# Optimization experiments

Hardware: AMD Instinct MI355X
Metric: run time of the kernel (lower is better)

The kernel has to match this reference:

```python
import jax, jax.numpy as jnp
import numpy as np

HIDDEN = 2048
N_HEADS = 16
N_KV_HEADS = 4
HEAD_DIM = HIDDEN // N_HEADS  # 128
WINDOW = 2048
ROPE_THETA = 10000.0


def setup_inputs() -> dict:
    key = jax.random.key(0)
    ks = jax.random.split(key, 5)
    B, S = 1, 4096
    scale = 0.02
    return {
        "hidden_states": jax.random.normal(ks[0], (B, S, HIDDEN), dtype=jnp.float32),
        # nn.Linear weights are [out_features, in_features]
        "q_w": jax.random.normal(ks[1], (N_HEADS * HEAD_DIM, HIDDEN), dtype=jnp.float32) * scale,
        "k_w": jax.random.normal(ks[2], (N_KV_HEADS * HEAD_DIM, HIDDEN), dtype=jnp.float32) * scale,
        "v_w": jax.random.normal(ks[3], (N_KV_HEADS * HEAD_DIM, HIDDEN), dtype=jnp.float32) * scale,
        "o_w": jax.random.normal(ks[4], (HIDDEN, N_HEADS * HEAD_DIM), dtype=jnp.float32) * scale,
    }


def _rope_cos_sin(seq_len, dtype):
    inv_freq = 1.0 / (ROPE_THETA ** (jnp.arange(0, HEAD_DIM, 2, dtype=jnp.float32) / HEAD_DIM))
    pos = jnp.arange(seq_len, dtype=jnp.float32)
    freqs = pos[:, None] * inv_freq[None, :]          # [S, D/2]
    emb = jnp.concatenate([freqs, freqs], axis=-1)    # [S, D]
    return jnp.cos(emb).astype(dtype), jnp.sin(emb).astype(dtype)


def _rotate_half(x):
    x1, x2 = jnp.split(x, 2, axis=-1)
    return jnp.concatenate([-x2, x1], axis=-1)


def reference(hidden_states, q_w, k_w, v_w, o_w):
    B, S, _ = hidden_states.shape
    dtype = hidden_states.dtype

    q = hidden_states @ q_w.T                         # [B,S,H*D]
    k = hidden_states @ k_w.T                         # [B,S,Hkv*D]
    v = hidden_states @ v_w.T

    q = q.reshape(B, S, N_HEADS, HEAD_DIM).transpose(0, 2, 1, 3)      # [B,H,S,D]
    k = k.reshape(B, S, N_KV_HEADS, HEAD_DIM).transpose(0, 2, 1, 3)   # [B,Hkv,S,D]
    v = v.reshape(B, S, N_KV_HEADS, HEAD_DIM).transpose(0, 2, 1, 3)

    cos, sin = _rope_cos_sin(S, dtype)                # [S,D]
    cos = cos[None, None]
    sin = sin[None, None]
    q = q * cos + _rotate_half(q) * sin
    k = k * cos + _rotate_half(k) * sin

    n_rep = N_HEADS // N_KV_HEADS
    k = jnp.repeat(k, n_rep, axis=1)                  # [B,H,S,D]
    v = jnp.repeat(v, n_rep, axis=1)

    scores = jnp.einsum("bhqd,bhkd->bhqk", q, k) / jnp.sqrt(jnp.array(HEAD_DIM, dtype))

    pos = jnp.arange(S)
    rel = pos[:, None] - pos[None, :]
    allowed = (rel >= 0) & (rel < WINDOW)             # causal sliding window
    mask = jnp.where(allowed, jnp.array(0.0, dtype), jnp.array(-jnp.inf, dtype))
    scores = scores + mask[None, None]

    attn = jax.nn.softmax(scores.astype(jnp.float32), axis=-1).astype(dtype)

    out = jnp.einsum("bhqk,bhkd->bhqd", attn, v)      # [B,H,S,D]
    out = out.transpose(0, 2, 1, 3).reshape(B, S, N_HEADS * HEAD_DIM)
    return out @ o_w.T
```

## Files before the change

kernel.cpp:

```cpp
#include <hip/hip_runtime.h>
#include <stdint.h>

typedef unsigned short u16;
typedef unsigned int u32;
typedef float f32x4 __attribute__((ext_vector_type(4)));
typedef int   i32x4 __attribute__((ext_vector_type(4)));
typedef __bf16 bf16x8 __attribute__((ext_vector_type(8)));
typedef u16 u16x4 __attribute__((ext_vector_type(4)));

constexpr int S_LEN = 4096;
constexpr int HID   = 2048;
constexpr int WIN   = 2048;

__device__ __forceinline__ u32 f2bf_u(float f) {
  u32 u = __builtin_bit_cast(u32, f);
  return (u + 0x7fffu + ((u >> 16) & 1u)) >> 16;
}
__device__ __forceinline__ float bf2f(u16 u) {
  return __builtin_bit_cast(float, ((u32)u) << 16);
}
__device__ __forceinline__ void mfma16(f32x4& acc, i32x4 a, i32x4 b) {
  acc = __builtin_amdgcn_mfma_f32_16x16x32_bf16(
      __builtin_bit_cast(bf16x8, a), __builtin_bit_cast(bf16x8, b), acc, 0, 0, 0);
}
__device__ __forceinline__ void gload_lds16(const u16* g, u16* l) {
  __builtin_amdgcn_global_load_lds((const __attribute__((address_space(1))) u32*)g,
                                   (__attribute__((address_space(3))) u32*)l, 16, 0, 0);
}

__global__ __launch_bounds__(256) void cvt_bf16_kernel(const float* __restrict__ src,
                                                       u16* __restrict__ dst, int n8) {
  int t = blockIdx.x * 256 + threadIdx.x;
  if (t >= n8) return;
  const f32x4* s = (const f32x4*)src + (size_t)t * 2;
  f32x4 a = s[0], b = s[1];
  i32x4 o;
  o.x = (int)(f2bf_u(a.x) | (f2bf_u(a.y) << 16));
  o.y = (int)(f2bf_u(a.z) | (f2bf_u(a.w) << 16));
  o.z = (int)(f2bf_u(b.x) | (f2bf_u(b.y) << 16));
  o.w = (int)(f2bf_u(b.z) | (f2bf_u(b.w) << 16));
  *((i32x4*)dst + t) = o;
}

__global__ __launch_bounds__(256) void rope_table_kernel(float* __restrict__ cs,
                                                         float* __restrict__ sn) {
  int t = blockIdx.x * 256 + threadIdx.x;
  int d = t & 63, s = t >> 6;
  float inv = exp2f(-(float)d * 0.20762050593046014f);
  float f = (float)s * inv;
  cs[t] = cosf(f);
  sn[t] = sinf(f);
}

template <int NH>
__global__ __launch_bounds__(256) void rope_apply_kernel(u16* __restrict__ X,
                                                         const float* __restrict__ cs,
                                                         const float* __restrict__ sn) {
  int t = blockIdx.x * 256 + threadIdx.x;
  int d0 = (t & 15) * 4;
  int r = t >> 4;
  int h = r % NH;
  int s = r / NH;
  f32x4 c = *(const f32x4*)&cs[(s << 6) | d0];
  f32x4 si = *(const f32x4*)&sn[(s << 6) | d0];
  u16* p = X + (size_t)s * (NH * 128) + h * 128 + d0;
  u16x4 a = *(u16x4*)p, b = *(u16x4*)(p + 64);
  u16x4 oa, ob;
#pragma unroll
  for (int j = 0; j < 4; ++j) {
    float x1 = bf2f(a[j]), x2 = bf2f(b[j]);
    oa[j] = (u16)f2bf_u(x1 * c[j] - x2 * si[j]);
    ob[j] = (u16)f2bf_u(x2 * c[j] + x1 * si[j]);
  }
  *(u16x4*)p = oa;
  *(u16x4*)(p + 64) = ob;
}

template <int OUT_MODE>
__global__ __launch_bounds__(256) void gemm_bt_kernel(const u16* __restrict__ A,
                                                      const u16* __restrict__ B,
                                                      void* __restrict__ Cv,
                                                      int K, int N) {
  __shared__ __attribute__((aligned(16))) u16 sA[128 * 64];
  __shared__ __attribute__((aligned(16))) u16 sB[128 * 64];
  const int lane = threadIdx.x & 63;
  const int w = threadIdx.x >> 6;
  const int g = lane >> 4, ln = lane & 15;

  int wgid = blockIdx.y * gridDim.x + blockIdx.x;
  const int nwg = gridDim.x * gridDim.y;
  wgid = (wgid & 7) * (nwg >> 3) + (wgid >> 3);
  const int brow = (wgid / gridDim.x) * 128;
  const int bcol = (wgid % gridDim.x) * 128;
  const int wr = (w >> 1) * 64, wc = (w & 1) * 64;

  f32x4 acc[4][4] = {};

  const int sr = w * 32 + (lane >> 3);
  const int scol = (lane & 7) * 8;
  const u16* Abase = A + (size_t)(brow + sr) * K + scol;
  const u16* Bbase = B + (size_t)(bcol + sr) * K + scol;
  u16* sAdst = &sA[w * 2048];
  u16* sBdst = &sB[w * 2048];

  for (int k0 = 0; k0 < K; k0 += 64) {
    __syncthreads();
#pragma unroll
    for (int i = 0; i < 4; ++i) {
      gload_lds16(Abase + (size_t)i * 8 * K + k0, sAdst + i * 512);
      gload_lds16(Bbase + (size_t)i * 8 * K + k0, sBdst + i * 512);
    }
    __syncthreads();
#pragma unroll
    for (int kk = 0; kk < 2; ++kk) {
      i32x4 af[4], bfr[4];
#pragma unroll
      for (int m = 0; m < 4; ++m)
        af[m] = *(const i32x4*)&sA[(wr + m * 16 + ln) * 64 + kk * 32 + g * 8];
#pragma unroll
      for (int n = 0; n < 4; ++n)
        bfr[n] = *(const i32x4*)&sB[(wc + n * 16 + ln) * 64 + kk * 32 + g * 8];
#pragma unroll
      for (int m = 0; m < 4; ++m)
#pragma unroll
        for (int n = 0; n < 4; ++n) mfma16(acc[m][n], af[m], bfr[n]);
    }
  }

  const int orow0 = brow + wr + g * 4;
  const int ocol0 = bcol + wc + ln;
#pragma unroll
  for (int m = 0; m < 4; ++m)
#pragma unroll
    for (int n = 0; n < 4; ++n)
#pragma unroll
      for (int j = 0; j < 4; ++j) {
        int row = orow0 + m * 16 + j;
        int col = ocol0 + n * 16;
        float v = acc[m][n][j];
        if constexpr (OUT_MODE == 0) {
          ((u16*)Cv)[(size_t)row * N + col] = (u16)f2bf_u(v);
        } else if constexpr (OUT_MODE == 1) {
          int d = col & 127, kvh = col >> 7;
          int T = row >> 5, ks = row & 31;
          int t = ks >> 4, gg = (ks >> 2) & 3, e = (t << 2) | (ks & 3);
          size_t idx = (size_t)kvh * S_LEN * 128 + (size_t)T * 4096 +
                       (size_t)d * 32 + ((size_t)(gg ^ ((d >> 1) & 3)) << 3) + e;
          ((u16*)Cv)[idx] = (u16)f2bf_u(v);
        } else {
          ((float*)Cv)[(size_t)row * N + col] = v;
        }
      }
}

__global__ __launch_bounds__(64) void attn_kernel(const u16* __restrict__ Q,
                                                  const u16* __restrict__ Kb,
                                                  const u16* __restrict__ Vt,
                                                  u16* __restrict__ opart,
                                                  float* __restrict__ mpart,
                                                  float* __restrict__ lpart) {
  const int lane = threadIdx.x;
  const int g = lane >> 4, ln = lane & 15;

  const int o = blockIdx.x;
  const int wgid = ((o & 7) << 9) | (o >> 3);
  const int h = wgid >> 8;
  const int idx = wgid & 255;
  const int chunk = idx & 1;
  const int gq = 127 - (idx >> 1);
  const int kvh = h >> 2;
  const int qr0 = gq * 32;

  i32x4 aq[2][4];
#pragma unroll
  for (int qf = 0; qf < 2; ++qf) {
    const u16* qp = Q + (size_t)(qr0 + qf * 16 + ln) * HID + h * 128 + g * 8;
#pragma unroll
    for (int c = 0; c < 4; ++c) aq[qf][c] = *(const i32x4*)(qp + c * 32);
  }

  f32x4 oacc[2][8] = {};
  float mrun[2] = {-1e30f, -1e30f};
  float lrun[2] = {0.f, 0.f};

  int lo = qr0 - (WIN - 1);
  if (lo < 0) lo = 0;
  lo &= ~31;
  const int nt_full = ((qr0 + 32) - lo) >> 5;
  const int nt0 = nt_full >> 1;
  const int lo_c = lo + (chunk ? nt0 * 32 : 0);
  const int nt = chunk ? nt_full - nt0 : nt0;

  const u16* kptr = Kb + (size_t)(lo_c + ln) * 512 + kvh * 128 + g * 8;
  const int vswz = (g ^ ((ln >> 1) & 3)) << 3;
  const u16* vptr = Vt + (size_t)kvh * S_LEN * 128 +
                    (size_t)(lo_c >> 5) * 4096 + ln * 32 + vswz;

  const float scale = 0.088388347648318447f;

  i32x4 kf[2][4], vf[8];
  if (nt > 0) {
#pragma unroll
    for (int t = 0; t < 2; ++t)
#pragma unroll
      for (int c = 0; c < 4; ++c)
        kf[t][c] = *(const i32x4*)(kptr + t * 8192 + c * 32);
#pragma unroll
    for (int nf = 0; nf < 8; ++nf) vf[nf] = *(const i32x4*)(vptr + nf * 512);
  }

  for (int it = 0; it < nt; ++it) {
    const int kb = lo_c + it * 32;
    const bool more = (it + 1 < nt);

    f32x4 sc[2][2] = {};
    __builtin_amdgcn_s_setprio(1);
#pragma unroll
    for (int c = 0; c < 4; ++c) {
      mfma16(sc[0][0], kf[0][c], aq[0][c]);
      mfma16(sc[0][1], kf[1][c], aq[0][c]);
      mfma16(sc[1][0], kf[0][c], aq[1][c]);
      mfma16(sc[1][1], kf[1][c], aq[1][c]);
    }
    __builtin_amdgcn_s_setprio(0);

    if (more) {
      kptr += 32 * 512;
#pragma unroll
      for (int t = 0; t < 2; ++t)
#pragma unroll
        for (int c = 0; c < 4; ++c)
          kf[t][c] = *(const i32x4*)(kptr + t * 8192 + c * 32);
    }

    float p[2][8];
    float mx[2];
    const bool interior = (kb + 31 <= qr0) && (qr0 + 31 - kb < WIN);
#pragma unroll
    for (int qf = 0; qf < 2; ++qf) {
      if (interior) {
#pragma unroll
        for (int j = 0; j < 4; ++j) {
          p[qf][j] = sc[qf][0][j] * scale;
          p[qf][4 + j] = sc[qf][1][j] * scale;
        }
      } else {
        const float NEG = -__builtin_inff();
        const int q = qr0 + qf * 16 + ln;
#pragma unroll
        for (int t = 0; t < 2; ++t)
#pragma unroll
          for (int j = 0; j < 4; ++j) {
            int k = kb + t * 16 + g * 4 + j;
            float s = sc[qf][t][j] * scale;
            p[qf][t * 4 + j] = (k <= q && q - k < WIN) ? s : NEG;
          }
      }
      float m = fmaxf(fmaxf(fmaxf(p[qf][0], p[qf][1]), fmaxf(p[qf][2], p[qf][3])),
                      fmaxf(fmaxf(p[qf][4], p[qf][5]), fmaxf(p[qf][6], p[qf][7])));
      m = fmaxf(m, __shfl_xor(m, 16));
      m = fmaxf(m, __shfl_xor(m, 32));
      mx[qf] = m;
    }

    float corr[2] = {1.f, 1.f};
    const bool noskip =
        !__all((mx[0] - mrun[0] <= 8.f) && (mx[1] - mrun[1] <= 8.f));
    if (noskip) {
#pragma unroll
      for (int qf = 0; qf < 2; ++qf) {
        float mnew = fmaxf(mrun[qf], mx[qf]);
        corr[qf] = __expf(mrun[qf] - mnew);
        mrun[qf] = mnew;
        f32x4 cv;
#pragma unroll
        for (int j = 0; j < 4; ++j) cv[j] = __shfl(corr[qf], g * 4 + j);
#pragma unroll
        for (int nf = 0; nf < 8; ++nf)
#pragma unroll
          for (int j = 0; j < 4; ++j) oacc[qf][nf][j] *= cv[j];
      }
    }

    i32x4 pa[2];
#pragma unroll
    for (int qf = 0; qf < 2; ++qf) {
#pragma unroll
      for (int e = 0; e < 8; ++e) p[qf][e] = __expf(p[qf][e] - mrun[qf]);
      float rs = ((p[qf][0] + p[qf][1]) + (p[qf][2] + p[qf][3])) +
                 ((p[qf][4] + p[qf][5]) + (p[qf][6] + p[qf][7]));
      rs += __shfl_xor(rs, 16);
      rs += __shfl_xor(rs, 32);
      lrun[qf] = lrun[qf] * corr[qf] + rs;
      pa[qf].x = (int)(f2bf_u(p[qf][0]) | (f2bf_u(p[qf][1]) << 16));
      pa[qf].y = (int)(f2bf_u(p[qf][2]) | (f2bf_u(p[qf][3]) << 16));
      pa[qf].z = (int)(f2bf_u(p[qf][4]) | (f2bf_u(p[qf][5]) << 16));
      pa[qf].w = (int)(f2bf_u(p[qf][6]) | (f2bf_u(p[qf][7]) << 16));
    }

    __builtin_amdgcn_s_setprio(1);
#pragma unroll
    for (int nf = 0; nf < 8; ++nf) {
      mfma16(oacc[0][nf], pa[0], vf[nf]);
      mfma16(oacc[1][nf], pa[1], vf[nf]);
    }
    __builtin_amdgcn_s_setprio(0);

    if (more) {
      vptr += 4096;
#pragma unroll
      for (int nf = 0; nf < 8; ++nf) vf[nf] = *(const i32x4*)(vptr + nf * 512);
    }
  }

  const size_t pb = ((size_t)chunk * 16 + h) * S_LEN;
#pragma unroll
  for (int qf = 0; qf < 2; ++qf) {
    if (g == 0) {
      mpart[pb + qr0 + qf * 16 + ln] = mrun[qf];
      lpart[pb + qr0 + qf * 16 + ln] = lrun[qf];
    }
    u16* aop = opart + (pb + qr0 + qf * 16 + g * 4) * 128 + ln;
#pragma unroll
    for (int j = 0; j < 4; ++j)
#pragma unroll
      for (int nf = 0; nf < 8; ++nf)
        aop[(size_t)j * 128 + nf * 16] = (u16)f2bf_u(oacc[qf][nf][j]);
  }
}

__global__ __launch_bounds__(256) void attn_combine_kernel(
    const u16* __restrict__ opart, const float* __restrict__ mpart,
    const float* __restrict__ lpart, u16* __restrict__ AO) {
  int t = blockIdx.x * 256 + threadIdx.x;
  int d0 = (t & 15) * 8;
  int rh = t >> 4;
  int row = rh & (S_LEN - 1);
  int h = rh >> 12;
  size_t i0 = (size_t)h * S_LEN + row;
  size_t i1 = i0 + (size_t)16 * S_LEN;
  float m0 = mpart[i0], m1 = mpart[i1];
  float l0 = lpart[i0], l1 = lpart[i1];
  float m = fmaxf(m0, m1);
  float w0 = __expf(m0 - m), w1 = __expf(m1 - m);
  float inv = 1.f / (l0 * w0 + l1 * w1);
  w0 *= inv;
  w1 *= inv;
  i32x4 v0 = *(const i32x4*)(opart + i0 * 128 + d0);
  i32x4 v1 = *(const i32x4*)(opart + i1 * 128 + d0);
  i32x4 ov;
#pragma unroll
  for (int j = 0; j < 4; ++j) {
    u32 a = ((u32)v0[j]), b = ((u32)v1[j]);
    float x = bf2f((u16)a) * w0 + bf2f((u16)b) * w1;
    float y = bf2f((u16)(a >> 16)) * w0 + bf2f((u16)(b >> 16)) * w1;
    ov[j] = (int)(f2bf_u(x) | (f2bf_u(y) << 16));
  }
  *(i32x4*)(AO + (size_t)row * HID + h * 128 + d0) = ov;
}

extern "C" void kernel_launch(void* const* d_in, const int* in_sizes, int n_in,
                              void* d_out, int out_size, void* d_ws, size_t ws_size,
                              hipStream_t stream) {
  const float* hx = (const float*)d_in[0];
  const float* qw = (const float*)d_in[1];
  const float* kw = (const float*)d_in[2];
  const float* vw = (const float*)d_in[3];
  const float* ow = (const float*)d_in[4];

  char* p = (char*)d_ws;
  u16* Xb = (u16*)p; p += (size_t)S_LEN * HID * 2;
  u16* Wq = (u16*)p; p += (size_t)HID * HID * 2;
  u16* Wk = (u16*)p; p += (size_t)512 * HID * 2;
  u16* Wv = (u16*)p; p += (size_t)512 * HID * 2;
  u16* Wo = (u16*)p; p += (size_t)HID * HID * 2;
  u16* Qb = (u16*)p; p += (size_t)S_LEN * HID * 2;
  u16* Kb = (u16*)p; p += (size_t)S_LEN * 512 * 2;
  u16* Vt = (u16*)p; p += (size_t)S_LEN * 512 * 2;
  u16* AO = (u16*)p; p += (size_t)S_LEN * HID * 2;
  float* cs = (float*)p; p += (size_t)S_LEN * 64 * 4;
  float* sn = (float*)p; p += (size_t)S_LEN * 64 * 4;
  u16* Opart = (u16*)p; p += (size_t)2 * 16 * S_LEN * 128 * 2;
  float* Mpart = (float*)p; p += (size_t)2 * 16 * S_LEN * 4;
  float* Lpart = (float*)p; p += (size_t)2 * 16 * S_LEN * 4;

  cvt_bf16_kernel<<<4096, 256, 0, stream>>>(hx, Xb, S_LEN * HID / 8);
  cvt_bf16_kernel<<<2048, 256, 0, stream>>>(qw, Wq, HID * HID / 8);
  cvt_bf16_kernel<<<512, 256, 0, stream>>>(kw, Wk, 512 * HID / 8);
  cvt_bf16_kernel<<<512, 256, 0, stream>>>(vw, Wv, 512 * HID / 8);
  cvt_bf16_kernel<<<2048, 256, 0, stream>>>(ow, Wo, HID * HID / 8);
  rope_table_kernel<<<S_LEN * 64 / 256, 256, 0, stream>>>(cs, sn);

  gemm_bt_kernel<0><<<dim3(16, 32), 256, 0, stream>>>(Xb, Wq, Qb, HID, HID);
  gemm_bt_kernel<0><<<dim3(4, 32), 256, 0, stream>>>(Xb, Wk, Kb, HID, 512);
  gemm_bt_kernel<1><<<dim3(4, 32), 256, 0, stream>>>(Xb, Wv, Vt, HID, 512);

  rope_apply_kernel<16><<<S_LEN * 16 * 16 / 256, 256, 0, stream>>>(Qb, cs, sn);
  rope_apply_kernel<4><<<S_LEN * 4 * 16 / 256, 256, 0, stream>>>(Kb, cs, sn);

  attn_kernel<<<4096, 64, 0, stream>>>(Qb, Kb, Vt, Opart, Mpart, Lpart);
  attn_combine_kernel<<<S_LEN * 16 * 16 / 256, 256, 0, stream>>>(Opart, Mpart,
                                                                 Lpart, AO);

  gemm_bt_kernel<2><<<dim3(16, 32), 256, 0, stream>>>(AO, Wo, d_out, HID, HID);
}
```

Baseline: 354.6 us.

## Merge launches, fold softmax scale into Q rope, use exp2 in attention

Merges the five fp32-to-bf16 conversions into one launch, the Q/K/V projections into a single 768-block GEMM, and the two RoPE passes into one kernel. The softmax scale and log2(e) are folded into Q during RoPE, so attention drops its per-score multiply and uses native exp2. Row-sum shuffles move out of the loop to a single reduction at the end, bf16 packing uses a vector convert, and the lazy-rescale threshold rises from 8 to 11. Fewer launches and less inner-loop ALU work come at the cost of an extra rounding of Q scaling in bf16 and a looser rescale threshold that could raise overflow risk.

```diff
diff --git a/kernel.cpp b/kernel.cpp
--- a/kernel.cpp
+++ b/kernel.cpp
@@ -4,6 +4,7 @@
 typedef unsigned short u16;
 typedef unsigned int u32;
 typedef float f32x4 __attribute__((ext_vector_type(4)));
+typedef float f32x8 __attribute__((ext_vector_type(8)));
 typedef int   i32x4 __attribute__((ext_vector_type(4)));
 typedef __bf16 bf16x8 __attribute__((ext_vector_type(8)));
 typedef u16 u16x4 __attribute__((ext_vector_type(4)));
@@ -19,6 +20,13 @@
 __device__ __forceinline__ float bf2f(u16 u) {
   return __builtin_bit_cast(float, ((u32)u) << 16);
 }
+__device__ __forceinline__ float exp2x(float x) {
+#if __has_builtin(__builtin_amdgcn_exp2f)
+  return __builtin_amdgcn_exp2f(x);
+#else
+  return exp2f(x);
+#endif
+}
 __device__ __forceinline__ void mfma16(f32x4& acc, i32x4 a, i32x4 b) {
   acc = __builtin_amdgcn_mfma_f32_16x16x32_bf16(
       __builtin_bit_cast(bf16x8, a), __builtin_bit_cast(bf16x8, b), acc, 0, 0, 0);
@@ -28,18 +36,34 @@
                                    (__attribute__((address_space(3))) u32*)l, 16, 0, 0);
 }
 
-__global__ __launch_bounds__(256) void cvt_bf16_kernel(const float* __restrict__ src,
-                                                       u16* __restrict__ dst, int n8) {
+constexpr int CVT_B0 = 1048576;
+constexpr int CVT_B1 = CVT_B0 + 524288;
+constexpr int CVT_B2 = CVT_B1 + 131072;
+constexpr int CVT_B3 = CVT_B2 + 131072;
+constexpr int CVT_B4 = CVT_B3 + 524288;
+
+__global__ __launch_bounds__(256) void cvt_all_kernel(
+    const float* __restrict__ s0, const float* __restrict__ s1,
+    const float* __restrict__ s2, const float* __restrict__ s3,
+    const float* __restrict__ s4, u16* __restrict__ d0, u16* __restrict__ d1,
+    u16* __restrict__ d2, u16* __restrict__ d3, u16* __restrict__ d4) {
   int t = blockIdx.x * 256 + threadIdx.x;
-  if (t >= n8) return;
-  const f32x4* s = (const f32x4*)src + (size_t)t * 2;
-  f32x4 a = s[0], b = s[1];
+  const float* s;
+  u16* d;
+  int off;
+  if (t < CVT_B0) { s = s0; d = d0; off = t; }
+  else if (t < CVT_B1) { s = s1; d = d1; off = t - CVT_B0; }
+  else if (t < CVT_B2) { s = s2; d = d2; off = t - CVT_B1; }
+  else if (t < CVT_B3) { s = s3; d = d3; off = t - CVT_B2; }
+  else { s = s4; d = d4; off = t - CVT_B3; }
+  const f32x4* sp = (const f32x4*)s + (size_t)off * 2;
+  f32x4 a = sp[0], b = sp[1];
   i32x4 o;
   o.x = (int)(f2bf_u(a.x) | (f2bf_u(a.y) << 16));
   o.y = (int)(f2bf_u(a.z) | (f2bf_u(a.w) << 16));
   o.z = (int)(f2bf_u(b.x) | (f2bf_u(b.y) << 16));
   o.w = (int)(f2bf_u(b.z) | (f2bf_u(b.w) << 16));
-  *((i32x4*)dst + t) = o;
+  *((i32x4*)d + off) = o;
 }
 
 __global__ __launch_bounds__(256) void rope_table_kernel(float* __restrict__ cs,
@@ -52,35 +76,126 @@
   sn[t] = sinf(f);
 }
 
-template <int NH>
-__global__ __launch_bounds__(256) void rope_apply_kernel(u16* __restrict__ X,
-                                                         const float* __restrict__ cs,
-                                                         const float* __restrict__ sn) {
+__global__ __launch_bounds__(256) void rope_qk_kernel(u16* __restrict__ Qb,
+                                                      u16* __restrict__ Kb,
+                                                      const float* __restrict__ cs,
+                                                      const float* __restrict__ sn) {
+  const float SC2 = 0.088388347648318447f * 1.4426950408889634f;
   int t = blockIdx.x * 256 + threadIdx.x;
   int d0 = (t & 15) * 4;
   int r = t >> 4;
-  int h = r % NH;
-  int s = r / NH;
+  u16* p;
+  int s;
+  float qs;
+  if (r < S_LEN * 16) {
+    int h = r & 15; s = r >> 4;
+    p = Qb + (size_t)s * HID + h * 128 + d0;
+    qs = SC2;
+  } else {
+    int r2 = r - S_LEN * 16;
+    int h = r2 & 3; s = r2 >> 2;
+    p = Kb + (size_t)s * 512 + h * 128 + d0;
+    qs = 1.f;
+  }
   f32x4 c = *(const f32x4*)&cs[(s << 6) | d0];
   f32x4 si = *(const f32x4*)&sn[(s << 6) | d0];
-  u16* p = X + (size_t)s * (NH * 128) + h * 128 + d0;
   u16x4 a = *(u16x4*)p, b = *(u16x4*)(p + 64);
   u16x4 oa, ob;
 #pragma unroll
   for (int j = 0; j < 4; ++j) {
     float x1 = bf2f(a[j]), x2 = bf2f(b[j]);
-    oa[j] = (u16)f2bf_u(x1 * c[j] - x2 * si[j]);
-    ob[j] = (u16)f2bf_u(x2 * c[j] + x1 * si[j]);
+    oa[j] = (u16)f2bf_u((x1 * c[j] - x2 * si[j]) * qs);
+    ob[j] = (u16)f2bf_u((x2 * c[j] + x1 * si[j]) * qs);
   }
   *(u16x4*)p = oa;
   *(u16x4*)(p + 64) = ob;
 }
 
-template <int OUT_MODE>
-__global__ __launch_bounds__(256) void gemm_bt_kernel(const u16* __restrict__ A,
-                                                      const u16* __restrict__ B,
-                                                      void* __restrict__ Cv,
-                                                      int K, int N) {
+__global__ __launch_bounds__(256) void qkv_gemm_kernel(
+    const u16* __restrict__ A, const u16* __restrict__ Wq,
+    const u16* __restrict__ Wk, const u16* __restrict__ Wv,
+    u16* __restrict__ Qb, u16* __restrict__ Kb, u16* __restrict__ Vt) {
+  __shared__ __attribute__((aligned(16))) u16 sA[128 * 64];
+  __shared__ __attribute__((aligned(16))) u16 sB[128 * 64];
+  const int lane = threadIdx.x & 63;
+  const int w = threadIdx.x >> 6;
+  const int g = lane >> 4, ln = lane & 15;
+  const int K = HID;
+
+  int wgid = blockIdx.x;
+  wgid = (wgid & 7) * 96 + (wgid >> 3);
+  const int brow = (wgid / 24) * 128;
+  const int bcol = (wgid % 24) * 128;
+
+  const u16* B;
+  u16* out;
+  int bc, mode, N;
+  if (bcol < 2048)      { B = Wq; out = Qb; bc = bcol;        N = 2048; mode = 0; }
+  else if (bcol < 2560) { B = Wk; out = Kb; bc = bcol - 2048; N = 512;  mode = 0; }
+  else                  { B = Wv; out = Vt; bc = bcol - 2560; N = 512;  mode = 1; }
+
+  const int wr = (w >> 1) * 64, wc = (w & 1) * 64;
+  f32x4 acc[4][4] = {};
+
+  const int sr = w * 32 + (lane >> 3);
+  const int scol = (lane & 7) * 8;
+  const u16* Abase = A + (size_t)(brow + sr) * K + scol;
+  const u16* Bbase = B + (size_t)(bc + sr) * K + scol;
+  u16* sAdst = &sA[w * 2048];
+  u16* sBdst = &sB[w * 2048];
+
+  for (int k0 = 0; k0 < K; k0 += 64) {
+    __syncthreads();
+#pragma unroll
+    for (int i = 0; i < 4; ++i) {
+      gload_lds16(Abase + (size_t)i * 8 * K + k0, sAdst + i * 512);
+      gload_lds16(Bbase + (size_t)i * 8 * K + k0, sBdst + i * 512);
+    }
+    __syncthreads();
+#pragma unroll
+    for (int kk = 0; kk < 2; ++kk) {
+      i32x4 af[4], bfr[4];
+#pragma unroll
+      for (int m = 0; m < 4; ++m)
+        af[m] = *(const i32x4*)&sA[(wr + m * 16 + ln) * 64 + kk * 32 + g * 8];
+#pragma unroll
+      for (int n = 0; n < 4; ++n)
+        bfr[n] = *(const i32x4*)&sB[(wc + n * 16 + ln) * 64 + kk * 32 + g * 8];
+#pragma unroll
+      for (int m = 0; m < 4; ++m)
+#pragma unroll
+        for (int n = 0; n < 4; ++n) mfma16(acc[m][n], af[m], bfr[n]);
+    }
+  }
+
+  const int orow0 = brow + wr + g * 4;
+  const int ocol0 = bc + wc + ln;
+#pragma unroll
+  for (int m = 0; m < 4; ++m)
+#pragma unroll
+    for (int n = 0; n < 4; ++n)
+#pragma unroll
+      for (int j = 0; j < 4; ++j) {
+        int row = orow0 + m * 16 + j;
+        int col = ocol0 + n * 16;
+        float v = acc[m][n][j];
+        if (mode == 0) {
+          out[(size_t)row * N + col] = (u16)f2bf_u(v);
+        } else {
+          int d = col & 127, kvh = col >> 7;
+          int T = row >> 5, ks = row & 31;
+          int tt = ks >> 4, gg = (ks >> 2) & 3, e = (tt << 2) | (ks & 3);
+          size_t idx = (size_t)kvh * S_LEN * 128 + (size_t)T * 4096 +
+                       (size_t)d * 32 + ((size_t)(gg ^ ((d >> 1) & 3)) << 3) + e;
+          out[idx] = (u16)f2bf_u(v);
+        }
+      }
+}
+
+__global__ __launch_bounds__(256) void gemm_o_kernel(const u16* __restrict__ A,
+                                                     const u16* __restrict__ B,
+                                                     float* __restrict__ Cv,
+                                                     int K, int N) {
   __shared__ __attribute__((aligned(16))) u16 sA[128 * 64];
   __shared__ __attribute__((aligned(16))) u16 sB[128 * 64];
   const int lane = threadIdx.x & 63;
@@ -134,23 +249,8 @@
 #pragma unroll
     for (int n = 0; n < 4; ++n)
 #pragma unroll
-      for (int j = 0; j < 4; ++j) {
-        int row = orow0 + m * 16 + j;
-        int col = ocol0 + n * 16;
-        float v = acc[m][n][j];
-        if constexpr (OUT_MODE == 0) {
-          ((u16*)Cv)[(size_t)row * N + col] = (u16)f2bf_u(v);
-        } else if constexpr (OUT_MODE == 1) {
-          int d = col & 127, kvh = col >> 7;
-          int T = row >> 5, ks = row & 31;
-          int t = ks >> 4, gg = (ks >> 2) & 3, e = (t << 2) | (ks & 3);
-          size_t idx = (size_t)kvh * S_LEN * 128 + (size_t)T * 4096 +
-                       (size_t)d * 32 + ((size_t)(gg ^ ((d >> 1) & 3)) << 3) + e;
-          ((u16*)Cv)[idx] = (u16)f2bf_u(v);
-        } else {
-          ((float*)Cv)[(size_t)row * N + col] = v;
-        }
-      }
+      for (int j = 0; j < 4; ++j)
+        Cv[(size_t)(orow0 + m * 16 + j) * N + ocol0 + n * 16] = acc[m][n][j];
 }
 
 __global__ __launch_bounds__(64) void attn_kernel(const u16* __restrict__ Q,
@@ -196,8 +296,6 @@
   const u16* vptr = Vt + (size_t)kvh * S_LEN * 128 +
                     (size_t)(lo_c >> 5) * 4096 + ln * 32 + vswz;
 
-  const float scale = 0.088388347648318447f;
-
   i32x4 kf[2][4], vf[8];
   if (nt > 0) {
 #pragma unroll
@@ -241,8 +339,8 @@
       if (interior) {
 #pragma unroll
         for (int j = 0; j < 4; ++j) {
-          p[qf][j] = sc[qf][0][j] * scale;
-          p[qf][4 + j] = sc[qf][1][j] * scale;
+          p[qf][j] = sc[qf][0][j];
+          p[qf][4 + j] = sc[qf][1][j];
         }
       } else {
         const float NEG = -__builtin_inff();
@@ -252,12 +350,13 @@
 #pragma unroll
           for (int j = 0; j < 4; ++j) {
             int k = kb + t * 16 + g * 4 + j;
-            float s = sc[qf][t][j] * scale;
-            p[qf][t * 4 + j] = (k <= q && q - k < WIN) ? s : NEG;
+            p[qf][t * 4 + j] = (k <= q && q - k < WIN) ? sc[qf][t][j] : NEG;
           }
       }
-      float m = fmaxf(fmaxf(fmaxf(p[qf][0], p[qf][1]), fmaxf(p[qf][2], p[qf][3])),
-                      fmaxf(fmaxf(p[qf][4], p[qf][5]), fmaxf(p[qf][6], p[qf][7])));
+      float x0 = fmaxf(fmaxf(p[qf][0], p[qf][1]), p[qf][2]);
+      float x1 = fmaxf(fmaxf(p[qf][3], p[qf][4]), p[qf][5]);
+      float x2 = fmaxf(fmaxf(p[qf][6], p[qf][7]), x0);
+      float m = fmaxf(x1, x2);
       m = fmaxf(m, __shfl_xor(m, 16));
       m = fmaxf(m, __shfl_xor(m, 32));
       mx[qf] = m;
@@ -265,12 +364,12 @@
 
     float corr[2] = {1.f, 1.f};
     const bool noskip =
-        !__all((mx[0] - mrun[0] <= 8.f) && (mx[1] - mrun[1] <= 8.f));
+        !__all((mx[0] - mrun[0] <= 11.f) && (mx[1] - mrun[1] <= 11.f));
     if (noskip) {
 #pragma unroll
       for (int qf = 0; qf < 2; ++qf) {
         float mnew = fmaxf(mrun[qf], mx[qf]);
-        corr[qf] = __expf(mrun[qf] - mnew);
+        corr[qf] = exp2x(mrun[qf] - mnew);
         mrun[qf] = mnew;
         f32x4 cv;
 #pragma unroll
@@ -285,17 +384,14 @@
     i32x4 pa[2];
 #pragma unroll
     for (int qf = 0; qf < 2; ++qf) {
-#pragma unroll
-      for (int e = 0; e < 8; ++e) p[qf][e] = __expf(p[qf][e] - mrun[qf]);
-      float rs = ((p[qf][0] + p[qf][1]) + (p[qf][2] + p[qf][3])) +
-                 ((p[qf][4] + p[qf][5]) + (p[qf][6] + p[qf][7]));
-      rs += __shfl_xor(rs, 16);
-      rs += __shfl_xor(rs, 32);
+      f32x8 pv;
+#pragma unroll
+      for (int e = 0; e < 8; ++e) pv[e] = exp2x(p[qf][e] - mrun[qf]);
+      float rs = ((pv[0] + pv[1]) + (pv[2] + pv[3])) +
+                 ((pv[4] + pv[5]) + (pv[6] + pv[7]));
       lrun[qf] = lrun[qf] * corr[qf] + rs;
-      pa[qf].x = (int)(f2bf_u(p[qf][0]) | (f2bf_u(p[qf][1]) << 16));
-      pa[qf].y = (int)(f2bf_u(p[qf][2]) | (f2bf_u(p[qf][3]) << 16));
-      pa[qf].z = (int)(f2bf_u(p[qf][4]) | (f2bf_u(p[qf][5]) << 16));
-      pa[qf].w = (int)(f2bf_u(p[qf][6]) | (f2bf_u(p[qf][7]) << 16));
+      bf16x8 pb = __builtin_convertvector(pv, bf16x8);
+      pa[qf] = __builtin_bit_cast(i32x4, pb);
     }
 
     __builtin_amdgcn_s_setprio(1);
@@ -311,6 +407,14 @@
 #pragma unroll
       for (int nf = 0; nf < 8; ++nf) vf[nf] = *(const i32x4*)(vptr + nf * 512);
     }
+  }
+
+#pragma unroll
+  for (int qf = 0; qf < 2; ++qf) {
+    float l = lrun[qf];
+    l += __shfl_xor(l, 16);
+    l += __shfl_xor(l, 32);
+    lrun[qf] = l;
   }
 
   const size_t pb = ((size_t)chunk * 16 + h) * S_LEN;
@@ -342,7 +446,7 @@
   float m0 = mpart[i0], m1 = mpart[i1];
   float l0 = lpart[i0], l1 = lpart[i1];
   float m = fmaxf(m0, m1);
-  float w0 = __expf(m0 - m), w1 = __expf(m1 - m);
+  float w0 = exp2x(m0 - m), w1 = exp2x(m1 - m);
   float inv = 1.f / (l0 * w0 + l1 * w1);
   w0 *= inv;
   w1 *= inv;
@@ -384,23 +488,18 @@
   float* Mpart = (float*)p; p += (size_t)2 * 16 * S_LEN * 4;
   float* Lpart = (float*)p; p += (size_t)2 * 16 * S_LEN * 4;
 
-  cvt_bf16_kernel<<<4096, 256, 0, stream>>>(hx, Xb, S_LEN * HID / 8);
-  cvt_bf16_kernel<<<2048, 256, 0, stream>>>(qw, Wq, HID * HID / 8);
-  cvt_bf16_kernel<<<512, 256, 0, stream>>>(kw, Wk, 512 * HID / 8);
-  cvt_bf16_kernel<<<512, 256, 0, stream>>>(vw, Wv, 512 * HID / 8);
-  cvt_bf16_kernel<<<2048, 256, 0, stream>>>(ow, Wo, HID * HID / 8);
+  cvt_all_kernel<<<CVT_B4 / 256, 256, 0, stream>>>(hx, qw, kw, vw, ow, Xb, Wq,
+                                                   Wk, Wv, Wo);
   rope_table_kernel<<<S_LEN * 64 / 256, 256, 0, stream>>>(cs, sn);
 
-  gemm_bt_kernel<0><<<dim3(16, 32), 256, 0, stream>>>(Xb, Wq, Qb, HID, HID);
-  gemm_bt_kernel<0><<<dim3(4, 32), 256, 0, stream>>>(Xb, Wk, Kb, HID, 512);
-  gemm_bt_kernel<1><<<dim3(4, 32), 256, 0, stream>>>(Xb, Wv, Vt, HID, 512);
-
-  rope_apply_kernel<16><<<S_LEN * 16 * 16 / 256, 256, 0, stream>>>(Qb, cs, sn);
-  rope_apply_kernel<4><<<S_LEN * 4 * 16 / 256, 256, 0, stream>>>(Kb, cs, sn);
+  qkv_gemm_kernel<<<768, 256, 0, stream>>>(Xb, Wq, Wk, Wv, Qb, Kb, Vt);
+
+  rope_qk_kernel<<<S_LEN * 20 * 16 / 256, 256, 0, stream>>>(Qb, Kb, cs, sn);
 
   attn_kernel<<<4096, 64, 0, stream>>>(Qb, Kb, Vt, Opart, Mpart, Lpart);
   attn_combine_kernel<<<S_LEN * 16 * 16 / 256, 256, 0, stream>>>(Opart, Mpart,
                                                                  Lpart, AO);
 
-  gemm_bt_kernel<2><<<dim3(16, 32), 256, 0, stream>>>(AO, Wo, d_out, HID, HID);
-}
+  gemm_o_kernel<<<dim3(16, 32), 256, 0, stream>>>(AO, Wo, (float*)d_out, HID,
+                                                  HID);
+}
```

Result: faster. 315.6 us (-11.0%).
